# Kernel optimization log

Hardware: AMD Instinct MI355X
Metric: run time of the kernel (lower is better)

Reference implementation:

```python
import jax, jax.numpy as jnp
import numpy as np

K = 3  # kernel_size

def _hamming2d(k):
    h = np.hamming(k)
    return (np.outer(h, h)).astype(np.float32)

def setup_inputs() -> dict:
    key = jax.random.key(0)
    k1, k2 = jax.random.split(key)
    x = jax.random.normal(k1, (8, 64, 128, 128), dtype=jnp.float32)
    W = jax.random.normal(k2, (9, 64, 3, 3), dtype=jnp.float32) * 0.001
    b = jnp.zeros((9,), dtype=jnp.float32)
    return {"x": x, "W": W, "b": b}

def reference(x, W, b):
    B, C, H, Wd = x.shape
    # filter generator: 3x3 conv, padding=1 -> (B, K*K, H, W)
    mask = jax.lax.conv_general_dilated(
        x, W, window_strides=(1, 1), padding=((1, 1), (1, 1)),
        dimension_numbers=("NCHW", "OIHW", "NCHW")) + b[None, :, None, None]
    # kernel normalizer: softmax over the K*K taps, hamming reweight, renormalize
    mask = jax.nn.softmax(mask, axis=1)
    ham = jnp.asarray(_hamming2d(K).reshape(-1))  # (K*K,)
    mask = mask * ham[None, :, None, None]
    mask = mask / jnp.sum(mask, axis=1, keepdims=True)
    # carafe (up=1): weighted sum of KxK shifted neighborhoods, reflect-padded.
    pad = K // 2
    xp = jnp.pad(x, ((0, 0), (0, 0), (pad, pad), (pad, pad)), mode="reflect")
    lowpass = jnp.zeros_like(x)
    for idx in range(K * K):
        i, j = divmod(idx, K)
        lowpass = lowpass + xp[:, :, i:i + H, j:j + Wd] * mask[:, idx:idx + 1]
    # highpass = x - lowpass; residual output = x + highpass
    return 2.0 * x - lowpass
```

## Files before the change

### kernel.cpp

```cpp
#include <hip/hip_runtime.h>
#include <hip/hip_bf16.h>


typedef __attribute__((ext_vector_type(8))) short short8;
typedef __attribute__((ext_vector_type(4))) float floatx4;
typedef __attribute__((ext_vector_type(4))) unsigned uint4v;
typedef __attribute__((ext_vector_type(2))) float float2v;

#define IH 128
#define IW 128
#define CCH 64
#define TSX 16
#define TSY 4
#define TPX 18
#define TPY 6
#define CSH 72

__device__ __forceinline__ unsigned short f2bf(float f) {
    unsigned u = __float_as_uint(f);
    u += 0x7FFFu + ((u >> 16) & 1u);
    return (unsigned short)(u >> 16);
}
__device__ __forceinline__ unsigned pkbf(float a, float b) {
    union { __hip_bfloat162 h; unsigned u; } cv;
    cv.h = __float22bfloat162_rn(float2{a, b});
    return cv.u;
}
__device__ __forceinline__ float2v unpk(unsigned u) {
    float2v r;
    r.x = __uint_as_float(u << 16);
    r.y = __uint_as_float(u & 0xFFFF0000u);
    return r;
}

__global__ void ahpf_prep(const float* __restrict__ Wg,
                          unsigned short* __restrict__ wsp)
{
    const int i = blockIdx.x * 256 + threadIdx.x;
    if (i >= 18 * 64) return;
    const int s = i >> 6, l = i & 63;
    const int fm = l & 15, fq = l >> 4;
    const int tap = s >> 1, cb = (s & 1) * 32 + fq * 8;
    short8 v = (short8)0;
    if (fm < 9) {
#pragma unroll
        for (int jj = 0; jj < 8; ++jj)
            v[jj] = (short)f2bf(Wg[fm * 576 + (cb + jj) * 9 + tap]);
    }
    ((short8*)wsp)[i] = v;
}

template <bool USE_WS>
__global__ __launch_bounds__(64, 3) void ahpf_kernel(
    const float* __restrict__ x, const float* __restrict__ Wg,
    const float* __restrict__ bias, float* __restrict__ out,
    const unsigned short* __restrict__ wsp)
{
    __shared__ __align__(16) unsigned short sx[TPY * TPX * CSH];

    const int lane = threadIdx.x;

    const unsigned flat = blockIdx.x;
    const unsigned nid  = (flat & 7u) * 256u + (flat >> 3);
    const int bx = nid & 7, by = (nid >> 3) & 31, bz = nid >> 8;

    const int ty0 = by * TSY;
    const int tx0 = bx * TSX;
    const size_t hw = (size_t)IH * IW;
    const float* xb = x + (size_t)bz * CCH * hw;

    const int fm = lane & 15;
    const int fq = lane >> 4;

    {
        int gx0 = tx0 - 4;
        if (gx0 < 0) gx0 = 0;
        if (gx0 > IW - 24) gx0 = IW - 24;
        const bool xlo = (bx == 0), xhi = (bx == 7);
        const int cg8 = lane & 7;
#pragma unroll 2
        for (int it = 0; it < 5; ++it) {
            const int s = it * 64 + lane;
            if (s >= TPY * 6 * 8) break;
            const int u = s >> 3;
            const int y = u / 6, xg = u - 6 * y;
            int gy = ty0 + y - 1;
            gy = gy < 0 ? -gy : (gy >= IH ? 2 * IH - 2 - gy : gy);
            const float* src = xb + (size_t)(cg8 * 8) * hw
                             + (size_t)gy * IW + gx0 + 4 * xg;
            float4 v[8];
#pragma unroll
            for (int jj = 0; jj < 8; ++jj)
                v[jj] = *(const float4*)(src + (size_t)jj * hw);
            const int xbase = gx0 + 4 * xg - tx0 + 1;
#pragma unroll
            for (int e = 0; e < 4; ++e) {
                const float fe[8] = {
                    ((const float*)&v[0])[e], ((const float*)&v[1])[e],
                    ((const float*)&v[2])[e], ((const float*)&v[3])[e],
                    ((const float*)&v[4])[e], ((const float*)&v[5])[e],
                    ((const float*)&v[6])[e], ((const float*)&v[7])[e]};
                uint4v pk;
                pk.x = pkbf(fe[0], fe[1]); pk.y = pkbf(fe[2], fe[3]);
                pk.z = pkbf(fe[4], fe[5]); pk.w = pkbf(fe[6], fe[7]);
                const int gxe = gx0 + 4 * xg + e;
                const int xx = xbase + e;
                if (xx >= 0 && xx < TPX)
                    *(uint4v*)&sx[(y * TPX + xx) * CSH + cg8 * 8] = pk;
                if (xlo && gxe == 1)
                    *(uint4v*)&sx[(y * TPX + 0) * CSH + cg8 * 8] = pk;
                if (xhi && gxe == 126)
                    *(uint4v*)&sx[(y * TPX + 17) * CSH + cg8 * 8] = pk;
            }
        }
    }

    short8 afr[18];
    if (USE_WS) {
        const short8* wf = (const short8*)wsp;
#pragma unroll
        for (int s = 0; s < 18; ++s) afr[s] = wf[s * 64 + lane];
    } else {
#pragma unroll
        for (int s = 0; s < 18; ++s) {
            short8 a = (short8)0;
            if (fm < 9) {
                const int tap = s >> 1, cb = (s & 1) * 32 + fq * 8;
                const float* wp = Wg + fm * 576 + tap;
#pragma unroll
                for (int jj = 0; jj < 8; ++jj)
                    a[jj] = (short)f2bf(wp[(cb + jj) * 9]);
            }
            afr[s] = a;
        }
    }
    float bq[4];
#pragma unroll
    for (int r = 0; r < 4; ++r) {
        const int t = fq * 4 + r;
        bq[r] = (t < 9) ? bias[t] : 0.0f;
    }
    __syncthreads();

    const bool border = (bx == 0) | (bx == 7) | (by == 0) | (by == 31);
    const int n = fm;

#pragma unroll 1
    for (int R = 0; R < TSY; ++R) {
        const int h = ty0 + R, w = tx0 + n;

        short8 bfr[18];
#pragma unroll
        for (int s = 0; s < 18; ++s) {
            const int tap = s >> 1;
            const int dy = tap / 3 - 1, dx = tap % 3 - 1;
            bfr[s] = *(const short8*)&sx[((R + 1 + dy) * TPX + (n + 1 + dx)) * CSH
                                         + (s & 1) * 32 + fq * 8];
        }

        floatx4 acc = {0.f, 0.f, 0.f, 0.f};
        if (border) {
#pragma unroll
            for (int s = 0; s < 18; ++s) {
                const int tap = s >> 1;
                const int dy = tap / 3 - 1, dx = tap % 3 - 1;
                const int hy = h + dy, wx = w + dx;
                short8 bb = bfr[s];
                if (hy < 0 || hy >= IH || wx < 0 || wx >= IW) bb = (short8)0;
                acc = __builtin_amdgcn_mfma_f32_16x16x32_bf16(afr[s], bb, acc, 0, 0, 0);
            }
        } else {
#pragma unroll
            for (int s = 0; s < 18; ++s)
                acc = __builtin_amdgcn_mfma_f32_16x16x32_bf16(afr[s], bfr[s], acc, 0, 0, 0);
        }

        auto hamt = [](int t) {
            const float a = (t / 3 == 1) ? 1.f : 0.08f;
            const float b = (t % 3 == 1) ? 1.f : 0.08f;
            return a * b;
        };
        const int nval = (fq < 2) ? 4 : (fq == 2 ? 1 : 0);
        float e0 = 0, e1 = 0, e2 = 0, e3 = 0, ssum = 0;
        if (nval >= 1) { e0 = __expf(acc[0] + bq[0]) * hamt(fq * 4 + 0); ssum += e0; }
        if (nval >= 4) { e1 = __expf(acc[1] + bq[1]) * hamt(fq * 4 + 1); ssum += e1;
                         e2 = __expf(acc[2] + bq[2]) * hamt(fq * 4 + 2); ssum += e2;
                         e3 = __expf(acc[3] + bq[3]) * hamt(fq * 4 + 3); ssum += e3; }
        ssum += __shfl_xor(ssum, 16);
        ssum += __shfl_xor(ssum, 32);
        const float inv = 1.0f / ssum;

        const unsigned p01 = pkbf(e0 * inv, e1 * inv);
        const unsigned p23 = pkbf(e2 * inv, e3 * inv);
        const unsigned q0 = (unsigned)__shfl((int)p01, n);
        const unsigned q1 = (unsigned)__shfl((int)p23, n);
        const unsigned q2 = (unsigned)__shfl((int)p01, 16 + n);
        const unsigned q3 = (unsigned)__shfl((int)p23, 16 + n);
        const unsigned q4 = (unsigned)__shfl((int)p01, 32 + n);
        float mk[9];
        { float2v m;
          m = unpk(q0); mk[0] = m.x; mk[1] = m.y;
          m = unpk(q1); mk[2] = m.x; mk[3] = m.y;
          m = unpk(q2); mk[4] = m.x; mk[5] = m.y;
          m = unpk(q3); mk[6] = m.x; mk[7] = m.y;
          mk[8] = unpk(q4).x; }

        float2v l[8];
#pragma unroll
        for (int q = 0; q < 8; ++q) l[q] = (float2v)0.f;
#pragma unroll
        for (int t = 0; t < 9; ++t) {
            const float mt = mk[t];
            const uint4v b0 = *(const uint4v*)&bfr[2 * t];
            const uint4v b1 = *(const uint4v*)&bfr[2 * t + 1];
#pragma unroll
            for (int q = 0; q < 4; ++q) {
                l[q]     += mt * unpk(b0[q]);
                l[q + 4] += mt * unpk(b1[q]);
            }
        }
        const uint4v c0 = *(const uint4v*)&bfr[8];
        const uint4v c1 = *(const uint4v*)&bfr[9];
        float* ob = out + (size_t)bz * CCH * hw + (size_t)h * IW + w
                  + (size_t)(8 * fq) * hw;
#pragma unroll
        for (int q = 0; q < 4; ++q) {
            const float2v oe = 2.f * unpk(c0[q]) - l[q];
            const float2v oo = 2.f * unpk(c1[q]) - l[q + 4];
            ob[(size_t)(2 * q) * hw]          = oe.x;
            ob[(size_t)(2 * q + 1) * hw]      = oe.y;
            ob[(size_t)(32 + 2 * q) * hw]     = oo.x;
            ob[(size_t)(32 + 2 * q + 1) * hw] = oo.y;
        }
    }
}

extern "C" void kernel_launch(void* const* d_in, const int* in_sizes, int n_in,
                              void* d_out, int out_size, void* d_ws, size_t ws_size,
                              hipStream_t stream) {
    const float* x    = (const float*)d_in[0];
    const float* Wg   = (const float*)d_in[1];
    const float* bias = (const float*)d_in[2];
    float* out        = (float*)d_out;
    const int B = in_sizes[0] / (CCH * IH * IW);
    const int nblk = B * 256;

    if (ws_size >= 18 * 64 * 16) {
        unsigned short* wsp = (unsigned short*)d_ws;
        ahpf_prep<<<5, 256, 0, stream>>>(Wg, wsp);
        ahpf_kernel<true><<<nblk, 64, 0, stream>>>(x, Wg, bias, out, wsp);
    } else {
        ahpf_kernel<false><<<nblk, 64, 0, stream>>>(x, Wg, bias, out, nullptr);
    }
}
```

Before: 118.0 us.

## Widen tiles to 32 columns, coalesce loads, stage output through LDS

Doubles the tile width to 32 columns and uses two waves per block, each computing two rows in 16-column halves. The input halo load changes from per-lane float4 gathers over eight channels to lane-per-column scalar loads over four channels, so reads are coalesced along a row. Outputs are staged in a padded shared buffer and written back as contiguous 32-float rows per channel instead of scattered per-lane stores. This adds LDS usage and an extra staging pass, and halves the block count.

```diff
diff --git a/kernel.cpp b/kernel.cpp
--- a/kernel.cpp
+++ b/kernel.cpp
@@ -5,14 +5,15 @@
 typedef __attribute__((ext_vector_type(8))) short short8;
 typedef __attribute__((ext_vector_type(4))) float floatx4;
 typedef __attribute__((ext_vector_type(4))) unsigned uint4v;
+typedef __attribute__((ext_vector_type(2))) unsigned uint2v;
 typedef __attribute__((ext_vector_type(2))) float float2v;
 
 #define IH 128
 #define IW 128
 #define CCH 64
-#define TSX 16
+#define TSX 32
 #define TSY 4
-#define TPX 18
+#define TPX 34
 #define TPY 6
 #define CSH 72
 
@@ -51,18 +52,21 @@
 }
 
 template <bool USE_WS>
-__global__ __launch_bounds__(64, 3) void ahpf_kernel(
+__global__ __launch_bounds__(128, 2) void ahpf_kernel(
     const float* __restrict__ x, const float* __restrict__ Wg,
     const float* __restrict__ bias, float* __restrict__ out,
     const unsigned short* __restrict__ wsp)
 {
     __shared__ __align__(16) unsigned short sx[TPY * TPX * CSH];
-
-    const int lane = threadIdx.x;
+    __shared__ __align__(16) float obuf[2 * 64 * 33];
+
+    const int tid  = threadIdx.x;
+    const int lane = tid & 63;
+    const int wv   = tid >> 6;
 
     const unsigned flat = blockIdx.x;
-    const unsigned nid  = (flat & 7u) * 256u + (flat >> 3);
-    const int bx = nid & 7, by = (nid >> 3) & 31, bz = nid >> 8;
+    const unsigned nid  = (flat & 7u) * 128u + (flat >> 3);
+    const int bx = nid & 3, by = (nid >> 2) & 31, bz = nid >> 7;
 
     const int ty0 = by * TSY;
     const int tx0 = bx * TSX;
@@ -73,45 +77,29 @@
     const int fq = lane >> 4;
 
     {
-        int gx0 = tx0 - 4;
-        if (gx0 < 0) gx0 = 0;
-        if (gx0 > IW - 24) gx0 = IW - 24;
-        const bool xlo = (bx == 0), xhi = (bx == 7);
-        const int cg8 = lane & 7;
+        const int gx0 = (bx == 0) ? 0 : (bx == 3 ? 64 : tx0 - 16);
+        const int gx  = gx0 + lane;
+        const int xx  = gx - tx0 + 1;
+        const bool in_tile = (xx >= 0) & (xx < TPX);
+        const bool xlo = (bx == 0) & (gx == 1);
+        const bool xhi = (bx == 3) & (gx == 126);
 #pragma unroll 2
-        for (int it = 0; it < 5; ++it) {
-            const int s = it * 64 + lane;
-            if (s >= TPY * 6 * 8) break;
-            const int u = s >> 3;
-            const int y = u / 6, xg = u - 6 * y;
+        for (int t = wv; t < 96; t += 2) {
+            const int cq = t & 15, y = t >> 4;
             int gy = ty0 + y - 1;
             gy = gy < 0 ? -gy : (gy >= IH ? 2 * IH - 2 - gy : gy);
-            const float* src = xb + (size_t)(cg8 * 8) * hw
-                             + (size_t)gy * IW + gx0 + 4 * xg;
-            float4 v[8];
-#pragma unroll
-            for (int jj = 0; jj < 8; ++jj)
-                v[jj] = *(const float4*)(src + (size_t)jj * hw);
-            const int xbase = gx0 + 4 * xg - tx0 + 1;
-#pragma unroll
-            for (int e = 0; e < 4; ++e) {
-                const float fe[8] = {
-                    ((const float*)&v[0])[e], ((const float*)&v[1])[e],
-                    ((const float*)&v[2])[e], ((const float*)&v[3])[e],
-                    ((const float*)&v[4])[e], ((const float*)&v[5])[e],
-                    ((const float*)&v[6])[e], ((const float*)&v[7])[e]};
-                uint4v pk;
-                pk.x = pkbf(fe[0], fe[1]); pk.y = pkbf(fe[2], fe[3]);
-                pk.z = pkbf(fe[4], fe[5]); pk.w = pkbf(fe[6], fe[7]);
-                const int gxe = gx0 + 4 * xg + e;
-                const int xx = xbase + e;
-                if (xx >= 0 && xx < TPX)
-                    *(uint4v*)&sx[(y * TPX + xx) * CSH + cg8 * 8] = pk;
-                if (xlo && gxe == 1)
-                    *(uint4v*)&sx[(y * TPX + 0) * CSH + cg8 * 8] = pk;
-                if (xhi && gxe == 126)
-                    *(uint4v*)&sx[(y * TPX + 17) * CSH + cg8 * 8] = pk;
-            }
+            const float* src = xb + (size_t)(4 * cq) * hw + (size_t)gy * IW + gx;
+            const float v0 = src[0];
+            const float v1 = src[hw];
+            const float v2 = src[2 * hw];
+            const float v3 = src[3 * hw];
+            uint2v pk;
+            pk.x = pkbf(v0, v1);
+            pk.y = pkbf(v2, v3);
+            const int rowb = y * TPX;
+            if (in_tile) *(uint2v*)&sx[(rowb + xx) * CSH + 4 * cq] = pk;
+            if (xlo)     *(uint2v*)&sx[(rowb +  0) * CSH + 4 * cq] = pk;
+            if (xhi)     *(uint2v*)&sx[(rowb + 33) * CSH + 4 * cq] = pk;
         }
     }
 
@@ -142,19 +130,23 @@
     }
     __syncthreads();
 
-    const bool border = (bx == 0) | (bx == 7) | (by == 0) | (by == 31);
+    const bool border = (bx == 0) | (bx == 3) | (by == 0) | (by == 31);
     const int n = fm;
+    float* ob_w = obuf + wv * (64 * 33);
 
 #pragma unroll 1
-    for (int R = 0; R < TSY; ++R) {
-        const int h = ty0 + R, w = tx0 + n;
+    for (int g = 0; g < 4; ++g) {
+        const int rl  = 2 * wv + (g >> 1);
+        const int cb  = (g & 1) * 16;
+        const int n16 = cb + n;
+        const int h   = ty0 + rl, w = tx0 + n16;
 
         short8 bfr[18];
 #pragma unroll
         for (int s = 0; s < 18; ++s) {
             const int tap = s >> 1;
             const int dy = tap / 3 - 1, dx = tap % 3 - 1;
-            bfr[s] = *(const short8*)&sx[((R + 1 + dy) * TPX + (n + 1 + dx)) * CSH
+            bfr[s] = *(const short8*)&sx[((rl + 1 + dy) * TPX + (n16 + 1 + dx)) * CSH
                                          + (s & 1) * 32 + fq * 8];
         }
 
@@ -221,16 +213,26 @@
         }
         const uint4v c0 = *(const uint4v*)&bfr[8];
         const uint4v c1 = *(const uint4v*)&bfr[9];
-        float* ob = out + (size_t)bz * CCH * hw + (size_t)h * IW + w
-                  + (size_t)(8 * fq) * hw;
 #pragma unroll
         for (int q = 0; q < 4; ++q) {
             const float2v oe = 2.f * unpk(c0[q]) - l[q];
             const float2v oo = 2.f * unpk(c1[q]) - l[q + 4];
-            ob[(size_t)(2 * q) * hw]          = oe.x;
-            ob[(size_t)(2 * q + 1) * hw]      = oe.y;
-            ob[(size_t)(32 + 2 * q) * hw]     = oo.x;
-            ob[(size_t)(32 + 2 * q + 1) * hw] = oo.y;
+            ob_w[(8 * fq + 2 * q)      * 33 + n16] = oe.x;
+            ob_w[(8 * fq + 2 * q + 1)  * 33 + n16] = oe.y;
+            ob_w[(32 + 8 * fq + 2 * q) * 33 + n16] = oo.x;
+            ob_w[(33 + 8 * fq + 2 * q) * 33 + n16] = oo.y;
+        }
+
+        if (g & 1) {
+            const int ci0 = lane >> 5;
+            const int col = lane & 31;
+            float* obase = out + (size_t)bz * CCH * hw
+                         + (size_t)h * IW + tx0 + col;
+#pragma unroll 8
+            for (int i = 0; i < 32; ++i) {
+                const int c = 2 * i + ci0;
+                obase[(size_t)c * hw] = ob_w[c * 33 + col];
+            }
         }
     }
 }
@@ -243,13 +245,13 @@
     const float* bias = (const float*)d_in[2];
     float* out        = (float*)d_out;
     const int B = in_sizes[0] / (CCH * IH * IW);
-    const int nblk = B * 256;
+    const int nblk = B * 128;
 
     if (ws_size >= 18 * 64 * 16) {
         unsigned short* wsp = (unsigned short*)d_ws;
         ahpf_prep<<<5, 256, 0, stream>>>(Wg, wsp);
-        ahpf_kernel<true><<<nblk, 64, 0, stream>>>(x, Wg, bias, out, wsp);
+        ahpf_kernel<true><<<nblk, 128, 0, stream>>>(x, Wg, bias, out, wsp);
     } else {
-        ahpf_kernel<false><<<nblk, 64, 0, stream>>>(x, Wg, bias, out, nullptr);
-    }
-}
+        ahpf_kernel<false><<<nblk, 128, 0, stream>>>(x, Wg, bias, out, nullptr);
+    }
+}
```

Result: slower. 144.1 us (+22.1%).
